# Optimization experiments

Hardware: AMD Instinct MI355X
Metric: run time of the kernel (lower is better)

## Reference

```python
import jax, jax.numpy as jnp
import numpy as np

N = 50000

def _gcn_norm(edge_index, n):
    src, dst = edge_index[0], edge_index[1]
    ones = jnp.ones(src.shape[0], dtype=jnp.float32)
    deg = jax.ops.segment_sum(ones, dst, num_segments=n) + 1.0  # +1 for self-loop
    dinv = deg ** -0.5
    norm = dinv[src] * dinv[dst]          # [E]
    inv_deg = 1.0 / deg                   # self-loop norm = deg^-1
    return src, dst, norm, inv_deg

def setup_inputs() -> dict:
    key = jax.random.key(0)
    ks = jax.random.split(key, 16)
    T, F, H = 12, 32, 64
    E = 1600000
    s = 0.05
    inp = {
        'x_seq': jax.random.normal(ks[0], (T, N, F), dtype=jnp.float32),
        'edge_index': jax.random.randint(ks[1], (2, E), 0, N, dtype=jnp.int32),
        'W1': jax.random.normal(ks[2], (F, H), dtype=jnp.float32) * s,
        'b1': jnp.zeros((H,), dtype=jnp.float32),
        'W2': jax.random.normal(ks[3], (H, H), dtype=jnp.float32) * s,
        'b2': jnp.zeros((H,), dtype=jnp.float32),
        'W_ih': jax.random.normal(ks[4], (3 * H, H), dtype=jnp.float32) * s,
        'W_hh': jax.random.normal(ks[5], (3 * H, H), dtype=jnp.float32) * s,
        'b_ih': jnp.zeros((3 * H,), dtype=jnp.float32),
        'b_hh': jnp.zeros((3 * H,), dtype=jnp.float32),
        'Wc1': jax.random.normal(ks[6], (H, H // 2), dtype=jnp.float32) * s,
        'bc1': jnp.zeros((H // 2,), dtype=jnp.float32),
        'Wc2': jax.random.normal(ks[7], (H // 2, 1), dtype=jnp.float32) * s,
        'bc2': jnp.zeros((1,), dtype=jnp.float32),
    }
    return inp

def _gcn_layer(h, W, b, src, dst, norm, inv_deg):
    h = jnp.einsum('tnf,fh->tnh', h, W)
    gathered = h[:, src, :] * norm[None, :, None]              # [T, E, H]
    seg = jax.vmap(lambda g: jax.ops.segment_sum(g, dst, num_segments=N))(gathered)
    return seg + h * inv_deg[None, :, None] + b

def _gru(temporal, W_ih, W_hh, b_ih, b_hh):
    # temporal: [T, N, H]; torch nn.GRU cell
    H = W_hh.shape[1]
    gi = jnp.einsum('tnh,gh->tng', temporal, W_ih) + b_ih       # precompute input gates
    h0 = jnp.zeros((temporal.shape[1], H), dtype=temporal.dtype)
    def step(h, gi_t):
        gh = h @ W_hh.T + b_hh
        i_r, i_z, i_n = jnp.split(gi_t, 3, axis=-1)
        h_r, h_z, h_n = jnp.split(gh, 3, axis=-1)
        r = jax.nn.sigmoid(i_r + h_r)
        z = jax.nn.sigmoid(i_z + h_z)
        n = jnp.tanh(i_n + r * h_n)
        h_new = (1.0 - z) * n + z * h
        return h_new, None
    h_last, _ = jax.lax.scan(step, h0, gi)
    return h_last

def reference(x_seq, edge_index, W1, b1, W2, b2, W_ih, W_hh, b_ih, b_hh, Wc1, bc1, Wc2, bc2):
    src, dst, norm, inv_deg = _gcn_norm(edge_index, N)
    h = x_seq
    h = jax.nn.relu(_gcn_layer(h, W1, b1, src, dst, norm, inv_deg))  # dropout is identity (eval)
    h = jax.nn.relu(_gcn_layer(h, W2, b2, src, dst, norm, inv_deg))
    h_last = _gru(h, W_ih, W_hh, b_ih, b_hh)                    # [N, H]
    hidden = jax.nn.relu(h_last @ Wc1 + bc1)
    logits = hidden @ Wc2 + bc2                                 # [N, 1]
    return logits
```

## Files before the change

### kernel.cpp

```cpp
#include <hip/hip_runtime.h>
#include <hip/hip_bf16.h>
#include <math.h>

#define NN 50000
#define TT 12
#define FF 32
#define HH 64

static inline size_t align256(size_t x){ return (x + 255) & ~(size_t)255; }


__global__ void k_count(const int* __restrict__ dst, int E, int* __restrict__ cnt){
  int i = blockIdx.x*blockDim.x + threadIdx.x;
  if (i < E) atomicAdd(&cnt[dst[i]], 1);
}

__global__ void k_dinv(const int* __restrict__ cnt, float* __restrict__ dinv,
                       float* __restrict__ invd, int n){
  int i = blockIdx.x*blockDim.x + threadIdx.x;
  if (i < n){
    float d = (float)(cnt[i] + 1);
    dinv[i] = (float)(1.0 / sqrt((double)d));
    invd[i] = 1.0f / d;
  }
}

#define SCAN_T 256
__global__ void k_scan(const int* __restrict__ cnt, int* __restrict__ rp, int n){
  __shared__ int s[SCAN_T];
  int t = threadIdx.x;
  int chunk = (n + SCAN_T - 1) / SCAN_T;
  int lo = t*chunk, hi = min(lo+chunk, n);
  int sum = 0;
  for (int i = lo; i < hi; ++i) sum += cnt[i];
  s[t] = sum; __syncthreads();
  for (int off = 1; off < SCAN_T; off <<= 1){
    int v = (t >= off) ? s[t-off] : 0;
    __syncthreads();
    s[t] += v;
    __syncthreads();
  }
  int run = (t == 0) ? 0 : s[t-1];
  for (int i = lo; i < hi; ++i){ rp[i] = run; run += cnt[i]; }
  if (t == SCAN_T-1) rp[n] = run;
}

__global__ void k_fill(const int* __restrict__ src, const int* __restrict__ dst, int E,
                       const int* __restrict__ rp, int* __restrict__ cur,
                       const float* __restrict__ dinv,
                       int* __restrict__ es, float* __restrict__ en){
  int i = blockIdx.x*blockDim.x + threadIdx.x;
  if (i < E){
    int d = dst[i], s = src[i];
    int pos = rp[d] + atomicAdd(&cur[d], 1);
    es[pos] = s;
    en[pos] = dinv[s] * dinv[d];
  }
}

__global__ void k_agg_x(const float* __restrict__ xt, const int* __restrict__ rp,
                        const int* __restrict__ es, const float* __restrict__ en,
                        const float* __restrict__ invd, float* __restrict__ out){
  int n = (blockIdx.x*blockDim.x + threadIdx.x) >> 5;
  if (n >= NN) return;
  int f = threadIdx.x & 31;
  float acc = invd[n] * xt[(size_t)n*FF + f];
  int e = rp[n], e1 = rp[n+1];
  for (; e + 4 <= e1; e += 4){
    int   s0 = es[e],   s1 = es[e+1], s2 = es[e+2], s3 = es[e+3];
    float w0 = en[e],   w1 = en[e+1], w2 = en[e+2], w3 = en[e+3];
    float v0 = xt[(size_t)s0*FF + f];
    float v1 = xt[(size_t)s1*FF + f];
    float v2 = xt[(size_t)s2*FF + f];
    float v3 = xt[(size_t)s3*FF + f];
    acc += w0*v0; acc += w1*v1; acc += w2*v2; acc += w3*v3;
  }
  for (; e < e1; ++e) acc += en[e] * xt[(size_t)es[e]*FF + f];
  out[(size_t)n*FF + f] = acc;
}

__global__ void k_agg_h(const float* __restrict__ h, const int* __restrict__ rp,
                        const int* __restrict__ es, const float* __restrict__ en,
                        const float* __restrict__ invd, float* __restrict__ out){
  int n = blockIdx.x*(blockDim.x >> 6) + (threadIdx.x >> 6);
  if (n >= NN) return;
  int lane = threadIdx.x & 63;
  float acc = invd[n] * h[(size_t)n*HH + lane];
  int e = rp[n], e1 = rp[n+1];
  for (; e + 4 <= e1; e += 4){
    int   s0 = es[e],   s1 = es[e+1], s2 = es[e+2], s3 = es[e+3];
    float w0 = en[e],   w1 = en[e+1], w2 = en[e+2], w3 = en[e+3];
    float v0 = h[(size_t)s0*HH + lane];
    float v1 = h[(size_t)s1*HH + lane];
    float v2 = h[(size_t)s2*HH + lane];
    float v3 = h[(size_t)s3*HH + lane];
    acc += w0*v0; acc += w1*v1; acc += w2*v2; acc += w3*v3;
  }
  for (; e < e1; ++e) acc += en[e] * h[(size_t)es[e]*HH + lane];
  out[(size_t)n*HH + lane] = acc;
}

template<int K, int ROWS, bool RELU>
__launch_bounds__(64)
__global__ void k_gemm(const float* __restrict__ A, const float* __restrict__ W,
                       const float* __restrict__ bias, float* __restrict__ C,
                       int M){
  int col = threadIdx.x;
  float w[K];
  #pragma unroll
  for (int k = 0; k < K; ++k) w[k] = W[(size_t)k*HH + col];
  float b = bias[col];
  int row0 = blockIdx.x*ROWS;
  if (row0 >= M) return;
  float acc[ROWS];
  #pragma unroll
  for (int r = 0; r < ROWS; ++r) acc[r] = b;
  #pragma unroll
  for (int r = 0; r < ROWS; ++r){
    const float* ar = A + (size_t)(row0 + r)*K;
    #pragma unroll
    for (int k = 0; k < K; ++k)
      acc[r] = fmaf(ar[k], w[k], acc[r]);
  }
  #pragma unroll
  for (int r = 0; r < ROWS; ++r){
    float v = acc[r];
    if (RELU) v = fmaxf(v, 0.f);
    C[(size_t)(row0 + r)*HH + col] = v;
  }
}

#define GRB 16
__launch_bounds__(384)
__global__ void k_gruf(const float* __restrict__ h2, const float* __restrict__ hprev,
                       const float* __restrict__ Wih, const float* __restrict__ Whh,
                       const float* __restrict__ bih, const float* __restrict__ bhh,
                       float* __restrict__ hnew, int ntiles){
  __shared__ float sh[2][GRB][64];
  __shared__ float ex[6][GRB][64];
  int tid = threadIdx.x, wv = tid >> 6, lane = tid & 63;
  int side = wv / 3;
  int gate = wv - side*3;
  const float* Wsel = side ? Whh : Wih;
  float bg = (side ? bhh : bih)[gate*64 + lane];
  float w[64];
  {
    const float* wr = Wsel + (size_t)(gate*64 + lane)*64;
    #pragma unroll
    for (int k = 0; k < 64; k += 4){
      float4 v = *(const float4*)(wr + k);
      w[k]=v.x; w[k+1]=v.y; w[k+2]=v.z; w[k+3]=v.w;
    }
  }

  for (int tile = blockIdx.x; tile < ntiles; tile += gridDim.x){
    int n0 = tile * GRB;
    __syncthreads();
    for (int i = tid; i < 2*GRB*16; i += 384){
      if (i < GRB*16) ((float4*)sh)[i] = ((const float4*)(h2    + (size_t)n0*64))[i];
      else            ((float4*)sh)[i] = ((const float4*)(hprev + (size_t)n0*64))[i - GRB*16];
    }
    __syncthreads();

    float a[GRB];
    #pragma unroll
    for (int r0 = 0; r0 < GRB; r0 += 4){
      const float* h0 = &sh[side][r0    ][0];
      const float* h1 = &sh[side][r0 + 1][0];
      const float* h2p= &sh[side][r0 + 2][0];
      const float* h3 = &sh[side][r0 + 3][0];
      float s0=0.f, s1=0.f, s2=0.f, s3=0.f;
      #pragma unroll
      for (int k = 0; k < 64; k += 4){
        float4 v0 = *(const float4*)(h0 + k);
        float4 v1 = *(const float4*)(h1 + k);
        float4 v2 = *(const float4*)(h2p + k);
        float4 v3 = *(const float4*)(h3 + k);
        s0 = fmaf(v0.x, w[k], s0); s0 = fmaf(v0.y, w[k+1], s0);
        s0 = fmaf(v0.z, w[k+2], s0); s0 = fmaf(v0.w, w[k+3], s0);
        s1 = fmaf(v1.x, w[k], s1); s1 = fmaf(v1.y, w[k+1], s1);
        s1 = fmaf(v1.z, w[k+2], s1); s1 = fmaf(v1.w, w[k+3], s1);
        s2 = fmaf(v2.x, w[k], s2); s2 = fmaf(v2.y, w[k+1], s2);
        s2 = fmaf(v2.z, w[k+2], s2); s2 = fmaf(v2.w, w[k+3], s2);
        s3 = fmaf(v3.x, w[k], s3); s3 = fmaf(v3.y, w[k+1], s3);
        s3 = fmaf(v3.z, w[k+2], s3); s3 = fmaf(v3.w, w[k+3], s3);
      }
      a[r0]=s0; a[r0+1]=s1; a[r0+2]=s2; a[r0+3]=s3;
    }
    #pragma unroll
    for (int r = 0; r < GRB; ++r) ex[wv][r][lane] = a[r] + bg;
    __syncthreads();
    for (int i = tid; i < GRB*64; i += 384){
      int row = i >> 6, col = i & 63;
      float ir = ex[0][row][col], iz = ex[1][row][col], in_ = ex[2][row][col];
      float hr = ex[3][row][col], hz = ex[4][row][col], hn  = ex[5][row][col];
      float rg = 1.f/(1.f + expf(-(ir + hr)));
      float zg = 1.f/(1.f + expf(-(iz + hz)));
      float nv = tanhf(in_ + rg*hn);
      float hp = sh[1][row][col];
      hnew[(size_t)(n0 + row)*64 + col] = (1.f - zg)*nv + zg*hp;
    }
  }
}

__global__ void k_head(const float* __restrict__ h, const float* __restrict__ Wc1,
                       const float* __restrict__ bc1, const float* __restrict__ Wc2,
                       const float* __restrict__ bc2, float* __restrict__ out){
  __shared__ float w1[64*32];
  __shared__ float w2[32];
  for (int i = threadIdx.x; i < 64*32; i += blockDim.x) w1[i] = Wc1[i];
  if (threadIdx.x < 32) w2[threadIdx.x] = Wc2[threadIdx.x];
  __syncthreads();
  int n = blockIdx.x*blockDim.x + threadIdx.x;
  if (n >= NN) return;
  const float* hr = h + (size_t)n*64;
  float hreg[64];
  #pragma unroll
  for (int k = 0; k < 64; ++k) hreg[k] = hr[k];
  float acc2 = bc2[0];
  #pragma unroll
  for (int c = 0; c < 32; ++c){
    float a = bc1[c];
    #pragma unroll
    for (int k = 0; k < 64; ++k) a = fmaf(hreg[k], w1[k*32 + c], a);
    a = fmaxf(a, 0.f);
    acc2 = fmaf(a, w2[c], acc2);
  }
  out[n] = acc2;
}

extern "C" void kernel_launch(void* const* d_in, const int* in_sizes, int n_in,
                              void* d_out, int out_size, void* d_ws, size_t ws_size,
                              hipStream_t stream){
  const float* x    = (const float*)d_in[0];
  const int*   ei   = (const int*)  d_in[1];
  const float* W1   = (const float*)d_in[2];
  const float* b1   = (const float*)d_in[3];
  const float* W2   = (const float*)d_in[4];
  const float* b2   = (const float*)d_in[5];
  const float* W_ih = (const float*)d_in[6];
  const float* W_hh = (const float*)d_in[7];
  const float* b_ih = (const float*)d_in[8];
  const float* b_hh = (const float*)d_in[9];
  const float* Wc1  = (const float*)d_in[10];
  const float* bc1  = (const float*)d_in[11];
  const float* Wc2  = (const float*)d_in[12];
  const float* bc2  = (const float*)d_in[13];
  int E = in_sizes[1] / 2;
  const int* src = ei;
  const int* dst = ei + E;

  char* w = (char*)d_ws;
  auto alloc = [&](size_t bytes){ char* p = w; w += align256(bytes); return p; };
  int*   cnt  = (int*)  alloc((size_t)NN*4);
  int*   rp   = (int*)  alloc((size_t)(NN+1)*4);
  int*   cur  = (int*)  alloc((size_t)NN*4);
  float* dinv = (float*)alloc((size_t)NN*4);
  float* invd = (float*)alloc((size_t)NN*4);
  int*   es   = (int*)  alloc((size_t)E*4);
  float* en   = (float*)alloc((size_t)E*4);
  float* U1   = (float*)alloc((size_t)NN*HH*4);
  float* U2   = (float*)alloc((size_t)NN*HH*4);
  float* hA   = (float*)alloc((size_t)NN*HH*4);
  float* hB   = (float*)alloc((size_t)NN*HH*4);
  if ((size_t)(w - (char*)d_ws) > ws_size) return;

  hipMemsetAsync(cnt, 0, (size_t)NN*4, stream);
  hipMemsetAsync(cur, 0, (size_t)NN*4, stream);
  hipMemsetAsync(hA,  0, (size_t)NN*HH*4, stream);

  k_count<<<(E+255)/256, 256, 0, stream>>>(dst, E, cnt);
  k_dinv <<<(NN+255)/256, 256, 0, stream>>>(cnt, dinv, invd, NN);
  k_scan <<<1, SCAN_T, 0, stream>>>(cnt, rp, NN);
  k_fill <<<(E+255)/256, 256, 0, stream>>>(src, dst, E, rp, cur, dinv, es, en);

  float* hprev = hA;
  float* hnext = hB;
  for (int t = 0; t < TT; ++t){
    const float* xt = x + (size_t)t*NN*FF;
    k_agg_x<<<(NN*32 + 255)/256, 256, 0, stream>>>(xt, rp, es, en, invd, U1);
    k_gemm<FF, 16, true><<<(NN + 15)/16, 64, 0, stream>>>(U1, W1, b1, U2, NN);
    k_agg_h<<<(NN + 3)/4, 256, 0, stream>>>(U2, rp, es, en, invd, U1);
    k_gemm<HH, 16, true><<<(NN + 15)/16, 64, 0, stream>>>(U1, W2, b2, U2, NN);
    k_gruf<<<1024, 384, 0, stream>>>(U2, hprev, W_ih, W_hh, b_ih, b_hh, hnext, NN/GRB);
    float* tmp = hprev; hprev = hnext; hnext = tmp;
  }

  k_head<<<(NN + 255)/256, 256, 0, stream>>>(hprev, Wc1, bc1, Wc2, bc2, (float*)d_out);
}
```

Baseline: 2.933 ms.

## Fuse GCN aggregation with dense transform and pack edge records

Merges each GCN layer's neighbour aggregation and its dense weight multiply plus ReLU into one kernel. Each wavefront handles one node, reduces neighbours into shared memory, then multiplies by the register-cached weight column. This drops two launches and two intermediate round-trips through global memory per timestep. Edge source index and normalisation weight are packed into one int2 record so each edge needs a single 8-byte load. In layer 1 the two half-wavefronts split the edge list and combine through shared memory with no barrier, which relies on wave-synchronous behaviour. Every block also reloads the weight column (32 to 64 registers per lane), which costs register pressure and redundant loads.

```diff
diff --git a/kernel.cpp b/kernel.cpp
--- a/kernel.cpp
+++ b/kernel.cpp
@@ -48,86 +48,100 @@
 __global__ void k_fill(const int* __restrict__ src, const int* __restrict__ dst, int E,
                        const int* __restrict__ rp, int* __restrict__ cur,
                        const float* __restrict__ dinv,
-                       int* __restrict__ es, float* __restrict__ en){
+                       int2* __restrict__ ef){
   int i = blockIdx.x*blockDim.x + threadIdx.x;
   if (i < E){
     int d = dst[i], s = src[i];
     int pos = rp[d] + atomicAdd(&cur[d], 1);
-    es[pos] = s;
-    en[pos] = dinv[s] * dinv[d];
-  }
-}
-
-__global__ void k_agg_x(const float* __restrict__ xt, const int* __restrict__ rp,
-                        const int* __restrict__ es, const float* __restrict__ en,
-                        const float* __restrict__ invd, float* __restrict__ out){
-  int n = (blockIdx.x*blockDim.x + threadIdx.x) >> 5;
+    int2 rec; rec.x = s; rec.y = __float_as_int(dinv[s] * dinv[d]);
+    ef[pos] = rec;
+  }
+}
+
+__launch_bounds__(256)
+__global__ void k_l1(const float* __restrict__ xt, const int* __restrict__ rp,
+                     const int2* __restrict__ ef, const float* __restrict__ invd,
+                     const float* __restrict__ W1, const float* __restrict__ b1,
+                     float* __restrict__ h1){
+  __shared__ float sh[4][2][32];
+  int wv = threadIdx.x >> 6, lane = threadIdx.x & 63;
+  int n = blockIdx.x*4 + wv;
   if (n >= NN) return;
-  int f = threadIdx.x & 31;
-  float acc = invd[n] * xt[(size_t)n*FF + f];
+  float w1c[32];
+  #pragma unroll
+  for (int k = 0; k < 32; ++k) w1c[k] = W1[k*64 + lane];
+  float bj = b1[lane];
+  int half = lane >> 5, f = lane & 31;
+
+  float acc = half ? 0.f : invd[n] * xt[(size_t)n*FF + f];
+  int e = rp[n] + half, e1 = rp[n+1];
+  for (; e + 2 < e1; e += 4){
+    int2 p = ef[e], q = ef[e+2];
+    acc = fmaf(__int_as_float(p.y), xt[(size_t)p.x*FF + f], acc);
+    acc = fmaf(__int_as_float(q.y), xt[(size_t)q.x*FF + f], acc);
+  }
+  if (e < e1){
+    int2 p = ef[e];
+    acc = fmaf(__int_as_float(p.y), xt[(size_t)p.x*FF + f], acc);
+  }
+  sh[wv][half][f] = acc;
+  if (lane < 32) sh[wv][0][f] = acc + sh[wv][1][f];
+  float hj = bj;
+  const float4* row = (const float4*)&sh[wv][0][0];
+  #pragma unroll
+  for (int i4 = 0; i4 < 8; ++i4){
+    float4 v = row[i4];
+    hj = fmaf(v.x, w1c[4*i4  ], hj);
+    hj = fmaf(v.y, w1c[4*i4+1], hj);
+    hj = fmaf(v.z, w1c[4*i4+2], hj);
+    hj = fmaf(v.w, w1c[4*i4+3], hj);
+  }
+  h1[(size_t)n*HH + lane] = fmaxf(hj, 0.f);
+}
+
+__launch_bounds__(256)
+__global__ void k_l2(const float* __restrict__ h1, const int* __restrict__ rp,
+                     const int2* __restrict__ ef, const float* __restrict__ invd,
+                     const float* __restrict__ W2, const float* __restrict__ b2,
+                     float* __restrict__ h2){
+  __shared__ float sh[4][64];
+  int wv = threadIdx.x >> 6, lane = threadIdx.x & 63;
+  int n = blockIdx.x*4 + wv;
+  if (n >= NN) return;
+  float w2c[64];
+  #pragma unroll
+  for (int k = 0; k < 64; ++k) w2c[k] = W2[k*64 + lane];
+  float bj = b2[lane];
+
+  float acc = invd[n] * h1[(size_t)n*HH + lane];
   int e = rp[n], e1 = rp[n+1];
   for (; e + 4 <= e1; e += 4){
-    int   s0 = es[e],   s1 = es[e+1], s2 = es[e+2], s3 = es[e+3];
-    float w0 = en[e],   w1 = en[e+1], w2 = en[e+2], w3 = en[e+3];
-    float v0 = xt[(size_t)s0*FF + f];
-    float v1 = xt[(size_t)s1*FF + f];
-    float v2 = xt[(size_t)s2*FF + f];
-    float v3 = xt[(size_t)s3*FF + f];
-    acc += w0*v0; acc += w1*v1; acc += w2*v2; acc += w3*v3;
-  }
-  for (; e < e1; ++e) acc += en[e] * xt[(size_t)es[e]*FF + f];
-  out[(size_t)n*FF + f] = acc;
-}
-
-__global__ void k_agg_h(const float* __restrict__ h, const int* __restrict__ rp,
-                        const int* __restrict__ es, const float* __restrict__ en,
-                        const float* __restrict__ invd, float* __restrict__ out){
-  int n = blockIdx.x*(blockDim.x >> 6) + (threadIdx.x >> 6);
-  if (n >= NN) return;
-  int lane = threadIdx.x & 63;
-  float acc = invd[n] * h[(size_t)n*HH + lane];
-  int e = rp[n], e1 = rp[n+1];
-  for (; e + 4 <= e1; e += 4){
-    int   s0 = es[e],   s1 = es[e+1], s2 = es[e+2], s3 = es[e+3];
-    float w0 = en[e],   w1 = en[e+1], w2 = en[e+2], w3 = en[e+3];
-    float v0 = h[(size_t)s0*HH + lane];
-    float v1 = h[(size_t)s1*HH + lane];
-    float v2 = h[(size_t)s2*HH + lane];
-    float v3 = h[(size_t)s3*HH + lane];
-    acc += w0*v0; acc += w1*v1; acc += w2*v2; acc += w3*v3;
-  }
-  for (; e < e1; ++e) acc += en[e] * h[(size_t)es[e]*HH + lane];
-  out[(size_t)n*HH + lane] = acc;
-}
-
-template<int K, int ROWS, bool RELU>
-__launch_bounds__(64)
-__global__ void k_gemm(const float* __restrict__ A, const float* __restrict__ W,
-                       const float* __restrict__ bias, float* __restrict__ C,
-                       int M){
-  int col = threadIdx.x;
-  float w[K];
-  #pragma unroll
-  for (int k = 0; k < K; ++k) w[k] = W[(size_t)k*HH + col];
-  float b = bias[col];
-  int row0 = blockIdx.x*ROWS;
-  if (row0 >= M) return;
-  float acc[ROWS];
-  #pragma unroll
-  for (int r = 0; r < ROWS; ++r) acc[r] = b;
-  #pragma unroll
-  for (int r = 0; r < ROWS; ++r){
-    const float* ar = A + (size_t)(row0 + r)*K;
-    #pragma unroll
-    for (int k = 0; k < K; ++k)
-      acc[r] = fmaf(ar[k], w[k], acc[r]);
-  }
-  #pragma unroll
-  for (int r = 0; r < ROWS; ++r){
-    float v = acc[r];
-    if (RELU) v = fmaxf(v, 0.f);
-    C[(size_t)(row0 + r)*HH + col] = v;
-  }
+    int2 p0 = ef[e], p1 = ef[e+1], p2 = ef[e+2], p3 = ef[e+3];
+    float v0 = h1[(size_t)p0.x*HH + lane];
+    float v1 = h1[(size_t)p1.x*HH + lane];
+    float v2 = h1[(size_t)p2.x*HH + lane];
+    float v3 = h1[(size_t)p3.x*HH + lane];
+    acc = fmaf(__int_as_float(p0.y), v0, acc);
+    acc = fmaf(__int_as_float(p1.y), v1, acc);
+    acc = fmaf(__int_as_float(p2.y), v2, acc);
+    acc = fmaf(__int_as_float(p3.y), v3, acc);
+  }
+  for (; e < e1; ++e){
+    int2 p = ef[e];
+    acc = fmaf(__int_as_float(p.y), h1[(size_t)p.x*HH + lane], acc);
+  }
+  sh[wv][lane] = acc;
+  float hj = bj;
+  const float4* row = (const float4*)&sh[wv][0];
+  #pragma unroll
+  for (int i4 = 0; i4 < 16; ++i4){
+    float4 v = row[i4];
+    hj = fmaf(v.x, w2c[4*i4  ], hj);
+    hj = fmaf(v.y, w2c[4*i4+1], hj);
+    hj = fmaf(v.z, w2c[4*i4+2], hj);
+    hj = fmaf(v.w, w2c[4*i4+3], hj);
+  }
+  h2[(size_t)n*HH + lane] = fmaxf(hj, 0.f);
 }
 
 #define GRB 16
@@ -166,14 +180,14 @@
     #pragma unroll
     for (int r0 = 0; r0 < GRB; r0 += 4){
       const float* h0 = &sh[side][r0    ][0];
-      const float* h1 = &sh[side][r0 + 1][0];
+      const float* h1p= &sh[side][r0 + 1][0];
       const float* h2p= &sh[side][r0 + 2][0];
       const float* h3 = &sh[side][r0 + 3][0];
       float s0=0.f, s1=0.f, s2=0.f, s3=0.f;
       #pragma unroll
       for (int k = 0; k < 64; k += 4){
         float4 v0 = *(const float4*)(h0 + k);
-        float4 v1 = *(const float4*)(h1 + k);
+        float4 v1 = *(const float4*)(h1p + k);
         float4 v2 = *(const float4*)(h2p + k);
         float4 v3 = *(const float4*)(h3 + k);
         s0 = fmaf(v0.x, w[k], s0); s0 = fmaf(v0.y, w[k+1], s0);
@@ -257,10 +271,9 @@
   int*   cur  = (int*)  alloc((size_t)NN*4);
   float* dinv = (float*)alloc((size_t)NN*4);
   float* invd = (float*)alloc((size_t)NN*4);
-  int*   es   = (int*)  alloc((size_t)E*4);
-  float* en   = (float*)alloc((size_t)E*4);
-  float* U1   = (float*)alloc((size_t)NN*HH*4);
-  float* U2   = (float*)alloc((size_t)NN*HH*4);
+  int2*  ef   = (int2*) alloc((size_t)E*8);
+  float* h1   = (float*)alloc((size_t)NN*HH*4);
+  float* h2   = (float*)alloc((size_t)NN*HH*4);
   float* hA   = (float*)alloc((size_t)NN*HH*4);
   float* hB   = (float*)alloc((size_t)NN*HH*4);
   if ((size_t)(w - (char*)d_ws) > ws_size) return;
@@ -272,17 +285,15 @@
   k_count<<<(E+255)/256, 256, 0, stream>>>(dst, E, cnt);
   k_dinv <<<(NN+255)/256, 256, 0, stream>>>(cnt, dinv, invd, NN);
   k_scan <<<1, SCAN_T, 0, stream>>>(cnt, rp, NN);
-  k_fill <<<(E+255)/256, 256, 0, stream>>>(src, dst, E, rp, cur, dinv, es, en);
+  k_fill <<<(E+255)/256, 256, 0, stream>>>(src, dst, E, rp, cur, dinv, ef);
 
   float* hprev = hA;
   float* hnext = hB;
   for (int t = 0; t < TT; ++t){
     const float* xt = x + (size_t)t*NN*FF;
-    k_agg_x<<<(NN*32 + 255)/256, 256, 0, stream>>>(xt, rp, es, en, invd, U1);
-    k_gemm<FF, 16, true><<<(NN + 15)/16, 64, 0, stream>>>(U1, W1, b1, U2, NN);
-    k_agg_h<<<(NN + 3)/4, 256, 0, stream>>>(U2, rp, es, en, invd, U1);
-    k_gemm<HH, 16, true><<<(NN + 15)/16, 64, 0, stream>>>(U1, W2, b2, U2, NN);
-    k_gruf<<<1024, 384, 0, stream>>>(U2, hprev, W_ih, W_hh, b_ih, b_hh, hnext, NN/GRB);
+    k_l1<<<(NN + 3)/4, 256, 0, stream>>>(xt, rp, ef, invd, W1, b1, h1);
+    k_l2<<<(NN + 3)/4, 256, 0, stream>>>(h1, rp, ef, invd, W2, b2, h2);
+    k_gruf<<<1024, 384, 0, stream>>>(h2, hprev, W_ih, W_hh, b_ih, b_hh, hnext, NN/GRB);
     float* tmp = hprev; hprev = hnext; hnext = tmp;
   }
 
```

Result: slower. 3.077 ms (+4.9%).
